# Kernel tuning notes

Hardware: AMD Instinct MI355X
Metric: run time of the kernel (lower is better)

## Reference

```python
import jax, jax.numpy as jnp
import numpy as np

EMB = 64
N_CONS = 100000
N_VARS = 200000
N_EDGES = 2000000


def _embed(x, shift, scale, W1, b1, W2, b2):
    # PreNormLayer (affine) -> Linear -> ReLU -> Linear -> ReLU
    x = (x - shift) * scale
    x = jax.nn.relu(x @ W1 + b1)
    return jax.nn.relu(x @ W2 + b2)


def _biconv(left, right, ei0, ei1, edge_lin, tgt_idx, n_tgt, tgt_feats,
            Wl, bl, Wr, sf, Wf, bf, sp, Woa, boa, Wob, bob):
    # gather-transform: per-edge joint features [E, EMB]
    joint = (left @ Wl + bl)[ei0] + edge_lin + (right @ Wr)[ei1]
    # feature_module_final: PreNorm(scale-only) -> ReLU -> Linear
    msg = jax.nn.relu(joint * sf) @ Wf + bf
    # scatter-add to target nodes, then post-conv PreNorm(scale-only)
    agg = jax.ops.segment_sum(msg, tgt_idx, num_segments=n_tgt) * sp
    h = jax.nn.relu(jnp.concatenate([agg, tgt_feats], axis=1) @ Woa + boa)
    return h @ Wob + bob


def _forward(constraint_features, edge_features, variable_features,
             c_shift, c_scale, c_W1, c_b1, c_W2, c_b2,
             v_shift, v_scale, v_W1, v_b1, v_W2, v_b2,
             e_shift, e_scale,
             vc_Wl, vc_bl, vc_We, vc_Wr, vc_sf, vc_Wf, vc_bf, vc_sp,
             vc_Woa, vc_boa, vc_Wob, vc_bob,
             cv_Wl, cv_bl, cv_We, cv_Wr, cv_sf, cv_Wf, cv_bf, cv_sp,
             cv_Woa, cv_boa, cv_Wob, cv_bob,
             out_W1, out_b1, out_W2, edge_indices):
    ei0, ei1 = edge_indices[0], edge_indices[1]
    c = _embed(constraint_features, c_shift, c_scale, c_W1, c_b1, c_W2, c_b2)
    v = _embed(variable_features, v_shift, v_scale, v_W1, v_b1, v_W2, v_b2)
    e = (edge_features - e_shift) * e_scale  # edge embedding = PreNorm only, dim 1
    # conv_v_to_c (right_to_left=True): target = constraints via ei0
    c = jax.nn.relu(_biconv(c, v, ei0, ei1, e @ vc_We, ei0, N_CONS, c,
                            vc_Wl, vc_bl, vc_Wr, vc_sf, vc_Wf, vc_bf, vc_sp,
                            vc_Woa, vc_boa, vc_Wob, vc_bob))
    # conv_c_to_v: target = variables via ei1
    v = jax.nn.relu(_biconv(c, v, ei0, ei1, e @ cv_We, ei1, N_VARS, v,
                            cv_Wl, cv_bl, cv_Wr, cv_sf, cv_Wf, cv_bf, cv_sp,
                            cv_Woa, cv_boa, cv_Wob, cv_bob))
    out = jax.nn.relu(v @ out_W1 + out_b1) @ out_W2  # [N_VARS, 1]
    return out.reshape(1, -1)


def setup_inputs():
    key = jax.random.key(0)
    ks = iter(jax.random.split(key, 64))

    def rn(shape, s=0.1):
        return (jax.random.normal(next(ks), shape, jnp.float32) * s).astype(jnp.float32)

    d = {}
    d["constraint_features"] = rn((N_CONS, 5), 1.0)
    d["edge_features"] = rn((N_EDGES, 1), 1.0)
    d["variable_features"] = rn((N_VARS, 19), 1.0)

    def prenorm(n, pre):
        d[pre + "shift"] = rn((n,), 0.05)
        d[pre + "scale"] = jnp.ones((n,), jnp.float32) + rn((n,), 0.05)

    prenorm(5, "c_"); prenorm(19, "v_"); prenorm(1, "e_")
    for pre, nin in (("c_", 5), ("v_", 19)):
        d[pre + "W1"] = rn((nin, EMB)); d[pre + "b1"] = rn((EMB,), 0.02)
        d[pre + "W2"] = rn((EMB, EMB)); d[pre + "b2"] = rn((EMB,), 0.02)
    for pre in ("vc_", "cv_"):
        d[pre + "Wl"] = rn((EMB, EMB)); d[pre + "bl"] = rn((EMB,), 0.02)
        d[pre + "We"] = rn((1, EMB)); d[pre + "Wr"] = rn((EMB, EMB))
        d[pre + "sf"] = jnp.float32(1.0) + rn((), 0.05)
        d[pre + "Wf"] = rn((EMB, EMB)); d[pre + "bf"] = rn((EMB,), 0.02)
        d[pre + "sp"] = jnp.float32(1.0) + rn((), 0.05)
        d[pre + "Woa"] = rn((2 * EMB, EMB)); d[pre + "boa"] = rn((EMB,), 0.02)
        d[pre + "Wob"] = rn((EMB, EMB)); d[pre + "bob"] = rn((EMB,), 0.02)
    d["out_W1"] = rn((EMB, EMB)); d["out_b1"] = rn((EMB,), 0.02)
    d["out_W2"] = rn((EMB, 1))
    d["edge_indices"] = jnp.stack([
        jax.random.randint(next(ks), (N_EDGES,), 0, N_CONS),
        jax.random.randint(next(ks), (N_EDGES,), 0, N_VARS)]).astype(jnp.int32)
    d["n_cons_per_sample"] = jnp.array([N_CONS], jnp.int32)
    d["n_vars_per_sample"] = jnp.array([N_VARS], jnp.int32)
    return d


def reference(constraint_features, edge_features, variable_features,
              c_shift, c_scale, c_W1, c_b1, c_W2, c_b2,
              v_shift, v_scale, v_W1, v_b1, v_W2, v_b2,
              e_shift, e_scale,
              vc_Wl, vc_bl, vc_We, vc_Wr, vc_sf, vc_Wf, vc_bf, vc_sp,
              vc_Woa, vc_boa, vc_Wob, vc_bob,
              cv_Wl, cv_bl, cv_We, cv_Wr, cv_sf, cv_Wf, cv_bf, cv_sp,
              cv_Woa, cv_boa, cv_Wob, cv_bob,
              out_W1, out_b1, out_W2,
              edge_indices, n_cons_per_sample, n_vars_per_sample):
    return _forward(constraint_features, edge_features, variable_features,
                    c_shift, c_scale, c_W1, c_b1, c_W2, c_b2,
                    v_shift, v_scale, v_W1, v_b1, v_W2, v_b2,
                    e_shift, e_scale,
                    vc_Wl, vc_bl, vc_We, vc_Wr, vc_sf, vc_Wf, vc_bf, vc_sp,
                    vc_Woa, vc_boa, vc_Wob, vc_bob,
                    cv_Wl, cv_bl, cv_We, cv_Wr, cv_sf, cv_Wf, cv_bf, cv_sp,
                    cv_Woa, cv_boa, cv_Wob, cv_bob,
                    out_W1, out_b1, out_W2, edge_indices)
```

## Files before the change

kernel.cpp:

```cpp
#include <hip/hip_runtime.h>
#include <hip/hip_bf16.h>

#define DEV __device__ __forceinline__

typedef __attribute__((ext_vector_type(8))) short short8;
typedef __attribute__((ext_vector_type(4))) float f32x4;

DEV unsigned short f2bf(float f) {
    __hip_bfloat16 h = __float2bfloat16(f);
    unsigned short u;
    __builtin_memcpy(&u, &h, 2);
    return u;
}
DEV float bf2f(unsigned short u) { return __uint_as_float((unsigned int)u << 16); }

DEV f32x4 mfma_bf16(short8 a, short8 b, f32x4 c) {
    return __builtin_amdgcn_mfma_f32_16x16x32_bf16(a, b, c, 0, 0, 0);
}

DEV void make_hilo(const float* a8, short8& hi, short8& lo) {
    #pragma unroll
    for (int j = 0; j < 8; ++j) {
        const float v = a8[j];
        const unsigned short h = f2bf(v);
        hi[j] = (short)h;
        lo[j] = (short)f2bf(v - bf2f(h));
    }
}

DEV void mfma3(f32x4 acc[4], short8 ah, short8 al,
               const unsigned short* __restrict__ Bh,
               const unsigned short* __restrict__ Bl,
               int nkt, int tidx, int lane) {
    #pragma unroll
    for (int c = 0; c < 4; ++c) {
        const size_t o = ((size_t)(c * nkt + tidx) * 64 + lane) * 8;
        const short8 bh = *(const short8*)(Bh + o);
        const short8 bl = *(const short8*)(Bl + o);
        acc[c] = mfma_bf16(ah, bh, acc[c]);
        acc[c] = mfma_bf16(al, bh, acc[c]);
        acc[c] = mfma_bf16(ah, bl, acc[c]);
    }
}

DEV int swf(int row, int col) {
    return row * 64 + ((((col >> 3) ^ row) & 7) << 3) + (col & 7);
}

DEV void gemm_lds(f32x4 acc[4], const float* Xl,
                  const unsigned short* Bh, const unsigned short* Bl,
                  int nkt, int t0, int ntk, int l15, int q, int lane) {
    for (int t = 0; t < ntk; ++t) {
        const int ch = (t * 4 + q) ^ (l15 & 7);
        const float* a8 = Xl + l15 * 64 + ch * 8;
        short8 ah, al;
        make_hilo(a8, ah, al);
        mfma3(acc, ah, al, Bh, Bl, nkt, t0 + t, lane);
    }
}

DEV void gemm_glb(f32x4 acc[4], const float* __restrict__ Xg, int rbase, int N,
                  const unsigned short* Bh, const unsigned short* Bl,
                  int nkt, int t0, int ntk, int l15, int q, int lane) {
    const int grow = rbase + l15;
    const bool ok = grow < N;
    for (int t = 0; t < ntk; ++t) {
        float a8[8];
        if (ok) {
            const float4 v0 = *(const float4*)(Xg + (size_t)grow * 64 + t * 32 + q * 8);
            const float4 v1 = *(const float4*)(Xg + (size_t)grow * 64 + t * 32 + q * 8 + 4);
            a8[0] = v0.x; a8[1] = v0.y; a8[2] = v0.z; a8[3] = v0.w;
            a8[4] = v1.x; a8[5] = v1.y; a8[6] = v1.z; a8[7] = v1.w;
        } else {
            #pragma unroll
            for (int j = 0; j < 8; ++j) a8[j] = 0.f;
        }
        short8 ah, al;
        make_hilo(a8, ah, al);
        mfma3(acc, ah, al, Bh, Bl, nkt, t0 + t, lane);
    }
}

#define NMAT 15
struct PrepArgs {
    const float* src[NMAT];
    unsigned short* hi[NMAT];
    unsigned short* lo[NMAT];
    int nkt[NMAT];
    int KR[NMAT];
};

__global__ __launch_bounds__(256)
void prep_kernel(PrepArgs pa)
{
    const int m = blockIdx.y;
    const int nkt = pa.nkt[m];
    const int nthr = nkt * 4 * 64;
    const int p = blockIdx.x * 256 + threadIdx.x;
    if (p >= nthr) return;
    const int f = p >> 6, l = p & 63;
    const int c = f / nkt, t = f % nkt;
    const int kbase = t * 32 + ((l >> 4) << 3);
    const int n = c * 16 + (l & 15);
    const float* W = pa.src[m];
    const int KR = pa.KR[m];
    unsigned short* ph = pa.hi[m] + (size_t)p * 8;
    unsigned short* pl = pa.lo[m] + (size_t)p * 8;
    #pragma unroll
    for (int j = 0; j < 8; ++j) {
        const int k = kbase + j;
        const float v = (k < KR) ? W[k * 64 + n] : 0.f;
        const unsigned short h = f2bf(v);
        ph[j] = h;
        pl[j] = f2bf(v - bf2f(h));
    }
}

struct FusedArgs {
    const int* ei; int E; int nH;
    int* h1; int* h2; unsigned int* rank;
    int tC, tV;
    const float* cf; int NC;
    const float* c_shift; const float* c_scale;
    const float* vf; int NV;
    const float* v_shift; const float* v_scale;
    const unsigned short *cW1h, *cW1l, *cW2h, *cW2l, *cWt1h, *cWt1l;
    const unsigned short *vW1h, *vW1l, *vW2h, *vW2l, *vWt1h, *vWt1l, *vWt2h, *vWt2l;
    const float *c_b1, *c_b2, *v_b1, *v_b2, *vc_bl;
    const float *vc_sf, *cv_sf;
    float* Emc; float* Emv;
    unsigned short* A1; unsigned short* B1; unsigned short* B2;
};

__global__ __launch_bounds__(256)
void fused_he_kernel(FusedArgs a)
{
    __shared__ __align__(16) float X0[4][16 * 32];
    __shared__ __align__(16) float Hb[4][1024];
    __shared__ __align__(16) float Eb[4][1024];

    const int half = blockIdx.x & 1;
    const int idx  = blockIdx.x >> 1;

    if (half == 0) {
        const int stride = a.nH * 256;
        for (int e = idx * 256 + (int)threadIdx.x; e < a.E; e += stride) {
            const int r1 = atomicAdd(a.h1 + a.ei[e], 1);
            const int r2 = atomicAdd(a.h2 + a.ei[a.E + e], 1);
            a.rank[e] = (unsigned int)r1 | ((unsigned int)r2 << 16);
        }
        return;
    }

    int tile = idx;
    const float* x; int N; int IN;
    const float *shift, *scale, *b1, *b2, *bt1;
    const unsigned short *W1h, *W1l, *W2h, *W2l, *Wt1h, *Wt1l;
    const unsigned short *Wt2h = nullptr, *Wt2l = nullptr;
    float* Em; unsigned short* T1; unsigned short* T2 = nullptr;
    float sf1, sf2 = 0.f;
    if (tile < a.tC) {
        x = a.cf; N = a.NC; IN = 5; shift = a.c_shift; scale = a.c_scale;
        W1h = a.cW1h; W1l = a.cW1l; b1 = a.c_b1;
        W2h = a.cW2h; W2l = a.cW2l; b2 = a.c_b2;
        Em = a.Emc; Wt1h = a.cWt1h; Wt1l = a.cWt1l; bt1 = a.vc_bl;
        sf1 = a.vc_sf[0]; T1 = a.A1;
    } else {
        tile -= a.tC;
        x = a.vf; N = a.NV; IN = 19; shift = a.v_shift; scale = a.v_scale;
        W1h = a.vW1h; W1l = a.vW1l; b1 = a.v_b1;
        W2h = a.vW2h; W2l = a.vW2l; b2 = a.v_b2;
        Em = a.Emv; Wt1h = a.vWt1h; Wt1l = a.vWt1l; bt1 = nullptr;
        sf1 = a.vc_sf[0]; T1 = a.B1;
        Wt2h = a.vWt2h; Wt2l = a.vWt2l; sf2 = a.cv_sf[0]; T2 = a.B2;
    }

    const int w = threadIdx.x >> 6, lane = threadIdx.x & 63;
    const int l15 = lane & 15, q = lane >> 4;
    const int rbase = tile * 64 + w * 16;

    #pragma unroll
    for (int i = 0; i < 8; ++i) {
        const int p = lane + 64 * i;
        const int row = p >> 5, col = p & 31;
        const int grow = rbase + row;
        float v = 0.f;
        if (grow < N && col < IN) v = (x[(size_t)grow * IN + col] - shift[col]) * scale[col];
        X0[w][row * 32 + (((col >> 3) ^ (row & 3)) << 3) + (col & 7)] = v;
    }

    {
        f32x4 acc[4] = {{0,0,0,0},{0,0,0,0},{0,0,0,0},{0,0,0,0}};
        const int ch = q ^ (l15 & 3);
        short8 ah, al;
        make_hilo(&X0[w][l15 * 32 + ch * 8], ah, al);
        mfma3(acc, ah, al, W1h, W1l, 1, 0, lane);
        #pragma unroll
        for (int c = 0; c < 4; ++c) {
            const int col = c * 16 + l15;
            const float bb = b1[col];
            #pragma unroll
            for (int r = 0; r < 4; ++r)
                Hb[w][swf(q * 4 + r, col)] = fmaxf(acc[c][r] + bb, 0.f);
        }
    }
    {
        f32x4 acc[4] = {{0,0,0,0},{0,0,0,0},{0,0,0,0},{0,0,0,0}};
        gemm_lds(acc, Hb[w], W2h, W2l, 2, 0, 2, l15, q, lane);
        #pragma unroll
        for (int c = 0; c < 4; ++c) {
            const int col = c * 16 + l15;
            const float bb = b2[col];
            #pragma unroll
            for (int r = 0; r < 4; ++r) {
                const int row = q * 4 + r;
                const int grow = rbase + row;
                const float v = fmaxf(acc[c][r] + bb, 0.f);
                Eb[w][swf(row, col)] = v;
                if (grow < N) Em[(size_t)grow * 64 + col] = v;
            }
        }
    }
    {
        f32x4 acc[4] = {{0,0,0,0},{0,0,0,0},{0,0,0,0},{0,0,0,0}};
        gemm_lds(acc, Eb[w], Wt1h, Wt1l, 2, 0, 2, l15, q, lane);
        #pragma unroll
        for (int c = 0; c < 4; ++c) {
            const int col = c * 16 + l15;
            const float bb = bt1 ? bt1[col] : 0.f;
            #pragma unroll
            for (int r = 0; r < 4; ++r) {
                const int grow = rbase + q * 4 + r;
                if (grow < N) T1[(size_t)grow * 64 + col] = f2bf(sf1 * (acc[c][r] + bb));
            }
        }
    }
    if (T2 != nullptr) {
        f32x4 acc[4] = {{0,0,0,0},{0,0,0,0},{0,0,0,0},{0,0,0,0}};
        gemm_lds(acc, Eb[w], Wt2h, Wt2l, 2, 0, 2, l15, q, lane);
        #pragma unroll
        for (int c = 0; c < 4; ++c) {
            const int col = c * 16 + l15;
            #pragma unroll
            for (int r = 0; r < 4; ++r) {
                const int grow = rbase + q * 4 + r;
                if (grow < N) T2[(size_t)grow * 64 + col] = f2bf(sf2 * acc[c][r]);
            }
        }
    }
}

template<bool IS_POST2>
__global__ __launch_bounds__(256)
void post_mfma(int N, const float* __restrict__ G, const int* __restrict__ rs,
               const float* __restrict__ Em,
               const unsigned short* __restrict__ Wfh, const unsigned short* __restrict__ Wfl,
               const float* __restrict__ bfv, const float* __restrict__ spp,
               const unsigned short* __restrict__ Woah, const unsigned short* __restrict__ Woal,
               const float* __restrict__ boa,
               const unsigned short* __restrict__ Wobh, const unsigned short* __restrict__ Wobl,
               const float* __restrict__ bob,
               const unsigned short* __restrict__ W4h, const unsigned short* __restrict__ W4l,
               const float* __restrict__ b4,
               const float* __restrict__ sf2p, unsigned short* __restrict__ A2,
               const float* __restrict__ oW2, float* __restrict__ out)
{
    __shared__ __align__(16) float BA[4][1024];
    __shared__ __align__(16) float BB[4][1024];

    const int w = threadIdx.x >> 6, lane = threadIdx.x & 63;
    const int l15 = lane & 15, q = lane >> 4;
    const float sp = spp[0];
    const float sf2 = IS_POST2 ? 0.f : sf2p[0];
    const int rbase = blockIdx.x * 64 + w * 16;

    {
        f32x4 acc[4] = {{0,0,0,0},{0,0,0,0},{0,0,0,0},{0,0,0,0}};
        gemm_glb(acc, G, rbase, N, Wfh, Wfl, 2, 0, 2, l15, q, lane);
        float dgr[4];
        #pragma unroll
        for (int r = 0; r < 4; ++r) {
            const int grow = rbase + q * 4 + r;
            dgr[r] = (grow < N) ? (float)(rs[grow + 1] - rs[grow]) : 0.f;
        }
        #pragma unroll
        for (int c = 0; c < 4; ++c) {
            const int col = c * 16 + l15;
            const float bb = bfv[col];
            #pragma unroll
            for (int r = 0; r < 4; ++r)
                BA[w][swf(q * 4 + r, col)] = (acc[c][r] + dgr[r] * bb) * sp;
        }
    }
    {
        f32x4 acc[4] = {{0,0,0,0},{0,0,0,0},{0,0,0,0},{0,0,0,0}};
        gemm_lds(acc, BA[w], Woah, Woal, 4, 0, 2, l15, q, lane);
        gemm_glb(acc, Em, rbase, N, Woah, Woal, 4, 2, 2, l15, q, lane);
        #pragma unroll
        for (int c = 0; c < 4; ++c) {
            const int col = c * 16 + l15;
            const float bb = boa[col];
            #pragma unroll
            for (int r = 0; r < 4; ++r)
                BB[w][swf(q * 4 + r, col)] = fmaxf(acc[c][r] + bb, 0.f);
        }
    }
    {
        f32x4 acc[4] = {{0,0,0,0},{0,0,0,0},{0,0,0,0},{0,0,0,0}};
        gemm_lds(acc, BB[w], Wobh, Wobl, 2, 0, 2, l15, q, lane);
        #pragma unroll
        for (int c = 0; c < 4; ++c) {
            const int col = c * 16 + l15;
            const float bb = bob[col];
            #pragma unroll
            for (int r = 0; r < 4; ++r)
                BA[w][swf(q * 4 + r, col)] = fmaxf(acc[c][r] + bb, 0.f);
        }
    }
    {
        f32x4 acc[4] = {{0,0,0,0},{0,0,0,0},{0,0,0,0},{0,0,0,0}};
        gemm_lds(acc, BA[w], W4h, W4l, 2, 0, 2, l15, q, lane);
        if (!IS_POST2) {
            #pragma unroll
            for (int c = 0; c < 4; ++c) {
                const int col = c * 16 + l15;
                const float bb = b4[col];
                #pragma unroll
                for (int r = 0; r < 4; ++r) {
                    const int grow = rbase + q * 4 + r;
                    if (grow < N) A2[(size_t)grow * 64 + col] = f2bf(sf2 * (acc[c][r] + bb));
                }
            }
        } else {
            float w2c[4], bb4[4];
            #pragma unroll
            for (int c = 0; c < 4; ++c) {
                const int col = c * 16 + l15;
                w2c[c] = oW2[col];
                bb4[c] = b4[col];
            }
            #pragma unroll
            for (int r = 0; r < 4; ++r) {
                float s = 0.f;
                #pragma unroll
                for (int c = 0; c < 4; ++c)
                    s += fmaxf(acc[c][r] + bb4[c], 0.f) * w2c[c];
                s += __shfl_xor(s, 1);
                s += __shfl_xor(s, 2);
                s += __shfl_xor(s, 4);
                s += __shfl_xor(s, 8);
                const int grow = rbase + q * 4 + r;
                if (l15 == 0 && grow < N) out[grow] = s;
            }
        }
    }
}

__global__ __launch_bounds__(256)
void scanA2_kernel(const int* __restrict__ h1, int n1, int* __restrict__ cs1,
                   const int* __restrict__ h2, int n2, int* __restrict__ cs2)
{
    __shared__ int wsum[4];
    const int which = blockIdx.y;
    const int* h = which ? h2 : h1;
    const int n = which ? n2 : n1;
    int* csum = which ? cs2 : cs1;
    if (blockIdx.x * 4096 >= n) return;

    const int t = threadIdx.x, lane = t & 63, wid = t >> 6;
    const int base = blockIdx.x * 4096 + t * 16;
    int s = 0;
    #pragma unroll
    for (int j = 0; j < 16; ++j) {
        const int idx = base + j;
        if (idx < n) s += h[idx];
    }
    #pragma unroll
    for (int d = 1; d < 64; d <<= 1) s += __shfl_xor(s, d);
    if (lane == 0) wsum[wid] = s;
    __syncthreads();
    if (t == 0) csum[blockIdx.x] = wsum[0] + wsum[1] + wsum[2] + wsum[3];
}

__global__ __launch_bounds__(256)
void scanB2_kernel(int* __restrict__ cs1, int nch1, int* __restrict__ rs1, int n1,
                   int* __restrict__ cs2, int nch2, int* __restrict__ rs2, int n2)
{
    __shared__ int wsum[4];
    const int which = blockIdx.x;
    int* csum = which ? cs2 : cs1;
    const int nchunks = which ? nch2 : nch1;
    int* rs = which ? rs2 : rs1;
    const int n = which ? n2 : n1;

    const int t = threadIdx.x, lane = t & 63, wid = t >> 6;
    const int v = (t < nchunks) ? csum[t] : 0;
    int x = v;
    #pragma unroll
    for (int d = 1; d < 64; d <<= 1) { int y = __shfl_up(x, d); if (lane >= d) x += y; }
    if (lane == 63) wsum[wid] = x;
    __syncthreads();
    int woff = 0;
    for (int i = 0; i < wid; ++i) woff += wsum[i];
    if (t < nchunks) csum[t] = woff + x - v;
    if (t == 0) rs[n] = wsum[0] + wsum[1] + wsum[2] + wsum[3];
}

__global__ __launch_bounds__(256)
void scanC2_kernel(const int* __restrict__ h1, int n1, const int* __restrict__ cs1,
                   int* __restrict__ rs1,
                   const int* __restrict__ h2, int n2, const int* __restrict__ cs2,
                   int* __restrict__ rs2)
{
    __shared__ int wsum[4];
    const int which = blockIdx.y;
    const int* h = which ? h2 : h1;
    const int n = which ? n2 : n1;
    const int* csum = which ? cs2 : cs1;
    int* rs = which ? rs2 : rs1;
    if (blockIdx.x * 4096 >= n) return;

    const int t = threadIdx.x, lane = t & 63, wid = t >> 6;
    const int base = blockIdx.x * 4096 + t * 16;
    int loc[16];
    int s = 0;
    #pragma unroll
    for (int j = 0; j < 16; ++j) {
        loc[j] = s;
        const int idx = base + j;
        if (idx < n) s += h[idx];
    }
    int x = s;
    #pragma unroll
    for (int d = 1; d < 64; d <<= 1) { int y = __shfl_up(x, d); if (lane >= d) x += y; }
    if (lane == 63) wsum[wid] = x;
    __syncthreads();
    int woff = 0;
    for (int i = 0; i < wid; ++i) woff += wsum[i];
    const int toff = csum[blockIdx.x] + woff + x - s;
    #pragma unroll
    for (int j = 0; j < 16; ++j) {
        const int idx = base + j;
        if (idx < n) rs[idx] = toff + loc[j];
    }
}

__global__ __launch_bounds__(256)
void scatter_kernel(const int* __restrict__ ei, int E,
                    const float* __restrict__ ef,
                    const float* __restrict__ eshp, const float* __restrict__ escp,
                    const unsigned int* __restrict__ rank,
                    const int* __restrict__ rs1, const int* __restrict__ rs2,
                    int2* __restrict__ pairs1, int2* __restrict__ pairs2)
{
    const int e = blockIdx.x * 256 + threadIdx.x;
    if (e >= E) return;
    const int i0 = ei[e];
    const int i1 = ei[E + e];
    const unsigned int rk = rank[e];
    const float en = (ef[e] - eshp[0]) * escp[0];
    const int enb = __float_as_int(en);
    const int pos1 = rs1[i0] + (int)(rk & 0xffffu);
    const int pos2 = rs2[i1] + (int)(rk >> 16);
    pairs1[pos1] = make_int2(i1, enb);
    pairs2[pos2] = make_int2(i0, enb);
}

__global__ __launch_bounds__(256)
void agg_kernel(int nrows, const int* __restrict__ rs,
                const int2* __restrict__ pairs,
                const unsigned short* __restrict__ Ttgt,
                const unsigned short* __restrict__ Tsrc,
                const float* __restrict__ We, const float* __restrict__ sfp,
                float* __restrict__ G)
{
    const int r = threadIdx.x >> 6;
    const int j = threadIdx.x & 63;
    const int row = blockIdx.x * 4 + r;
    if (row >= nrows) return;

    const float base = bf2f(Ttgt[(size_t)row * 64 + j]);
    const float sfWe = sfp[0] * We[j];
    const int s = rs[row];
    const int e = rs[row + 1];

    float acc = 0.f;
    int p = s;
    for (; p + 1 < e; p += 2) {
        const int2 pr0 = pairs[p];
        const int2 pr1 = pairs[p + 1];
        const float bs0 = bf2f(Tsrc[(size_t)pr0.x * 64 + j]);
        const float bs1 = bf2f(Tsrc[(size_t)pr1.x * 64 + j]);
        acc += fmaxf(base + bs0 + __int_as_float(pr0.y) * sfWe, 0.f);
        acc += fmaxf(base + bs1 + __int_as_float(pr1.y) * sfWe, 0.f);
    }
    if (p < e) {
        const int2 pr = pairs[p];
        const float bs = bf2f(Tsrc[(size_t)pr.x * 64 + j]);
        acc += fmaxf(base + bs + __int_as_float(pr.y) * sfWe, 0.f);
    }
    G[(size_t)row * 64 + j] = acc;
}

extern "C" void kernel_launch(void* const* d_in, const int* in_sizes, int n_in,
                              void* d_out, int out_size, void* d_ws, size_t ws_size,
                              hipStream_t stream)
{
    const float* cf      = (const float*)d_in[0];
    const float* ef      = (const float*)d_in[1];
    const float* vf      = (const float*)d_in[2];
    const float* c_shift = (const float*)d_in[3];
    const float* c_scale = (const float*)d_in[4];
    const float* v_shift = (const float*)d_in[5];
    const float* v_scale = (const float*)d_in[6];
    const float* e_shift = (const float*)d_in[7];
    const float* e_scale = (const float*)d_in[8];
    const float* c_W1 = (const float*)d_in[9];
    const float* c_b1 = (const float*)d_in[10];
    const float* c_W2 = (const float*)d_in[11];
    const float* c_b2 = (const float*)d_in[12];
    const float* v_W1 = (const float*)d_in[13];
    const float* v_b1 = (const float*)d_in[14];
    const float* v_W2 = (const float*)d_in[15];
    const float* v_b2 = (const float*)d_in[16];
    const float* vc_Wl  = (const float*)d_in[17];
    const float* vc_bl  = (const float*)d_in[18];
    const float* vc_We  = (const float*)d_in[19];
    const float* vc_Wr  = (const float*)d_in[20];
    const float* vc_sf  = (const float*)d_in[21];
    const float* vc_Wf  = (const float*)d_in[22];
    const float* vc_bf  = (const float*)d_in[23];
    const float* vc_sp  = (const float*)d_in[24];
    const float* vc_Woa = (const float*)d_in[25];
    const float* vc_boa = (const float*)d_in[26];
    const float* vc_Wob = (const float*)d_in[27];
    const float* vc_bob = (const float*)d_in[28];
    const float* cv_Wl  = (const float*)d_in[29];
    const float* cv_bl  = (const float*)d_in[30];
    const float* cv_We  = (const float*)d_in[31];
    const float* cv_Wr  = (const float*)d_in[32];
    const float* cv_sf  = (const float*)d_in[33];
    const float* cv_Wf  = (const float*)d_in[34];
    const float* cv_bf  = (const float*)d_in[35];
    const float* cv_sp  = (const float*)d_in[36];
    const float* cv_Woa = (const float*)d_in[37];
    const float* cv_boa = (const float*)d_in[38];
    const float* cv_Wob = (const float*)d_in[39];
    const float* cv_bob = (const float*)d_in[40];
    const float* out_W1 = (const float*)d_in[41];
    const float* out_b1 = (const float*)d_in[42];
    const float* out_W2 = (const float*)d_in[43];
    const int*   eidx   = (const int*)d_in[44];

    const int NC = in_sizes[0] / 5;
    const int NV = in_sizes[2] / 19;
    const int E  = in_sizes[1];

    char* ws = (char*)d_ws;
    size_t off = 0;
    auto alloc = [&](size_t bytes) -> size_t {
        size_t o = off;
        off = (off + bytes + 255) & ~(size_t)255;
        return o;
    };
    size_t o_h1 = alloc((size_t)NC * 4);
    size_t o_h2 = alloc((size_t)NV * 4);
    size_t zero_bytes = off;
    size_t o_rs1  = alloc((size_t)(NC + 1) * 4);
    size_t o_rs2  = alloc((size_t)(NV + 1) * 4);
    size_t o_cs1  = alloc(256 * 4);
    size_t o_cs2  = alloc(256 * 4);
    size_t o_p1   = alloc((size_t)E * 8);
    size_t o_p2   = alloc((size_t)E * 8);
    size_t o_G1   = alloc((size_t)NC * 64 * 4);
    size_t o_G2   = alloc((size_t)NV * 64 * 4);
    size_t o_Emc  = alloc((size_t)NC * 64 * 4);
    size_t o_Emv  = alloc((size_t)NV * 64 * 4);
    size_t o_A1   = alloc((size_t)NC * 64 * 2);
    size_t o_B1   = alloc((size_t)NV * 64 * 2);
    size_t o_B2   = alloc((size_t)NV * 64 * 2);

    static const int nkt_arr[NMAT] = {1,2,2,1,2,2,2,2,4,2,2,2,4,2,2};
    static const int KR_arr[NMAT]  = {5,64,64,19,64,64,64,64,128,64,64,64,128,64,64};
    const float* src_arr[NMAT] = {c_W1, c_W2, vc_Wl, v_W1, v_W2, vc_Wr, cv_Wr,
                                  vc_Wf, vc_Woa, vc_Wob, cv_Wl,
                                  cv_Wf, cv_Woa, cv_Wob, out_W1};
    size_t o_wh[NMAT], o_wl[NMAT];
    for (int m = 0; m < NMAT; ++m) {
        o_wh[m] = alloc((size_t)nkt_arr[m] * 4 * 64 * 8 * 2);
        o_wl[m] = alloc((size_t)nkt_arr[m] * 4 * 64 * 8 * 2);
    }
    (void)ws_size; (void)n_in; (void)out_size;

    int*  h1   = (int*)(ws + o_h1);
    int*  h2   = (int*)(ws + o_h2);
    int*  rs1  = (int*)(ws + o_rs1);
    int*  rs2  = (int*)(ws + o_rs2);
    int*  cs1  = (int*)(ws + o_cs1);
    int*  cs2  = (int*)(ws + o_cs2);
    unsigned int* rank = (unsigned int*)(ws + o_G1);
    int2* p1   = (int2*)(ws + o_p1);
    int2* p2   = (int2*)(ws + o_p2);
    float* G1  = (float*)(ws + o_G1);
    float* G2  = (float*)(ws + o_G2);
    float* Emc = (float*)(ws + o_Emc);
    float* Emv = (float*)(ws + o_Emv);
    unsigned short* A1 = (unsigned short*)(ws + o_A1);
    unsigned short* B1 = (unsigned short*)(ws + o_B1);
    unsigned short* A2 = (unsigned short*)(ws + o_A1);
    unsigned short* B2 = (unsigned short*)(ws + o_B2);

    PrepArgs pa;
    for (int m = 0; m < NMAT; ++m) {
        pa.src[m] = src_arr[m];
        pa.hi[m] = (unsigned short*)(ws + o_wh[m]);
        pa.lo[m] = (unsigned short*)(ws + o_wl[m]);
        pa.nkt[m] = nkt_arr[m];
        pa.KR[m] = KR_arr[m];
    }
    auto WH = [&](int m) { return (const unsigned short*)(ws + o_wh[m]); };
    auto WL = [&](int m) { return (const unsigned short*)(ws + o_wl[m]); };

    hipMemsetAsync(ws, 0, zero_bytes, stream);

    prep_kernel<<<dim3(4, NMAT), 256, 0, stream>>>(pa);

    const int tC = (NC + 63) >> 6, tV = (NV + 63) >> 6;
    const int nE = tC + tV;
    FusedArgs fa;
    fa.ei = eidx; fa.E = E; fa.nH = nE;
    fa.h1 = h1; fa.h2 = h2; fa.rank = rank;
    fa.tC = tC; fa.tV = tV;
    fa.cf = cf; fa.NC = NC; fa.c_shift = c_shift; fa.c_scale = c_scale;
    fa.vf = vf; fa.NV = NV; fa.v_shift = v_shift; fa.v_scale = v_scale;
    fa.cW1h = WH(0); fa.cW1l = WL(0); fa.cW2h = WH(1); fa.cW2l = WL(1);
    fa.cWt1h = WH(2); fa.cWt1l = WL(2);
    fa.vW1h = WH(3); fa.vW1l = WL(3); fa.vW2h = WH(4); fa.vW2l = WL(4);
    fa.vWt1h = WH(5); fa.vWt1l = WL(5); fa.vWt2h = WH(6); fa.vWt2l = WL(6);
    fa.c_b1 = c_b1; fa.c_b2 = c_b2; fa.v_b1 = v_b1; fa.v_b2 = v_b2;
    fa.vc_bl = vc_bl; fa.vc_sf = vc_sf; fa.cv_sf = cv_sf;
    fa.Emc = Emc; fa.Emv = Emv; fa.A1 = A1; fa.B1 = B1; fa.B2 = B2;
    fused_he_kernel<<<2 * nE, 256, 0, stream>>>(fa);

    const int nch1 = (NC + 4095) / 4096, nch2 = (NV + 4095) / 4096;
    const int nchm = nch1 > nch2 ? nch1 : nch2;
    scanA2_kernel<<<dim3(nchm, 2), 256, 0, stream>>>(h1, NC, cs1, h2, NV, cs2);
    scanB2_kernel<<<2, 256, 0, stream>>>(cs1, nch1, rs1, NC, cs2, nch2, rs2, NV);
    scanC2_kernel<<<dim3(nchm, 2), 256, 0, stream>>>(h1, NC, cs1, rs1, h2, NV, cs2, rs2);

    scatter_kernel<<<(E + 255) / 256, 256, 0, stream>>>(
        eidx, E, ef, e_shift, e_scale, rank, rs1, rs2, p1, p2);

    agg_kernel<<<(NC + 3) / 4, 256, 0, stream>>>(
        NC, rs1, p1, A1, B1, vc_We, vc_sf, G1);
    post_mfma<false><<<tC, 256, 0, stream>>>(
        NC, G1, rs1, Emc,
        WH(7), WL(7), vc_bf, vc_sp,
        WH(8), WL(8), vc_boa,
        WH(9), WL(9), vc_bob,
        WH(10), WL(10), cv_bl,
        cv_sf, A2, nullptr, nullptr);

    agg_kernel<<<(NV + 3) / 4, 256, 0, stream>>>(
        NV, rs2, p2, B2, A2, cv_We, cv_sf, G2);
    post_mfma<true><<<tV, 256, 0, stream>>>(
        NV, G2, rs2, Emv,
        WH(11), WL(11), cv_bf, cv_sp,
        WH(12), WL(12), cv_boa,
        WH(13), WL(13), cv_bob,
        WH(14), WL(14), out_b1,
        nullptr, nullptr, out_W2, (float*)d_out);
}
```

Baseline: 813.3 us.

## Split edge scatter and overlap second-direction scatter with first aggregation

```diff
diff --git a/kernel.cpp b/kernel.cpp
--- a/kernel.cpp
+++ b/kernel.cpp
@@ -135,9 +135,7 @@
 __global__ __launch_bounds__(256)
 void fused_he_kernel(FusedArgs a)
 {
-    __shared__ __align__(16) float X0[4][16 * 32];
-    __shared__ __align__(16) float Hb[4][1024];
-    __shared__ __align__(16) float Eb[4][1024];
+    __shared__ __align__(16) float Bb[4][1024];
 
     const int half = blockIdx.x & 1;
     const int idx  = blockIdx.x >> 1;
@@ -179,21 +177,19 @@
     const int l15 = lane & 15, q = lane >> 4;
     const int rbase = tile * 64 + w * 16;
 
-    #pragma unroll
-    for (int i = 0; i < 8; ++i) {
-        const int p = lane + 64 * i;
-        const int row = p >> 5, col = p & 31;
-        const int grow = rbase + row;
-        float v = 0.f;
-        if (grow < N && col < IN) v = (x[(size_t)grow * IN + col] - shift[col]) * scale[col];
-        X0[w][row * 32 + (((col >> 3) ^ (row & 3)) << 3) + (col & 7)] = v;
-    }
-
     {
         f32x4 acc[4] = {{0,0,0,0},{0,0,0,0},{0,0,0,0},{0,0,0,0}};
-        const int ch = q ^ (l15 & 3);
+        const int grow = rbase + l15;
+        float a8[8];
+        #pragma unroll
+        for (int j = 0; j < 8; ++j) {
+            const int col = q * 8 + j;
+            float v = 0.f;
+            if (grow < N && col < IN) v = (x[(size_t)grow * IN + col] - shift[col]) * scale[col];
+            a8[j] = v;
+        }
         short8 ah, al;
-        make_hilo(&X0[w][l15 * 32 + ch * 8], ah, al);
+        make_hilo(a8, ah, al);
         mfma3(acc, ah, al, W1h, W1l, 1, 0, lane);
         #pragma unroll
         for (int c = 0; c < 4; ++c) {
@@ -201,12 +197,12 @@
             const float bb = b1[col];
             #pragma unroll
             for (int r = 0; r < 4; ++r)
-                Hb[w][swf(q * 4 + r, col)] = fmaxf(acc[c][r] + bb, 0.f);
+                Bb[w][swf(q * 4 + r, col)] = fmaxf(acc[c][r] + bb, 0.f);
         }
     }
     {
         f32x4 acc[4] = {{0,0,0,0},{0,0,0,0},{0,0,0,0},{0,0,0,0}};
-        gemm_lds(acc, Hb[w], W2h, W2l, 2, 0, 2, l15, q, lane);
+        gemm_lds(acc, Bb[w], W2h, W2l, 2, 0, 2, l15, q, lane);
         #pragma unroll
         for (int c = 0; c < 4; ++c) {
             const int col = c * 16 + l15;
@@ -216,14 +212,14 @@
                 const int row = q * 4 + r;
                 const int grow = rbase + row;
                 const float v = fmaxf(acc[c][r] + bb, 0.f);
-                Eb[w][swf(row, col)] = v;
+                Bb[w][swf(row, col)] = v;
                 if (grow < N) Em[(size_t)grow * 64 + col] = v;
             }
         }
     }
     {
         f32x4 acc[4] = {{0,0,0,0},{0,0,0,0},{0,0,0,0},{0,0,0,0}};
-        gemm_lds(acc, Eb[w], Wt1h, Wt1l, 2, 0, 2, l15, q, lane);
+        gemm_lds(acc, Bb[w], Wt1h, Wt1l, 2, 0, 2, l15, q, lane);
         #pragma unroll
         for (int c = 0; c < 4; ++c) {
             const int col = c * 16 + l15;
@@ -237,7 +233,7 @@
     }
     if (T2 != nullptr) {
         f32x4 acc[4] = {{0,0,0,0},{0,0,0,0},{0,0,0,0},{0,0,0,0}};
-        gemm_lds(acc, Eb[w], Wt2h, Wt2l, 2, 0, 2, l15, q, lane);
+        gemm_lds(acc, Bb[w], Wt2h, Wt2l, 2, 0, 2, l15, q, lane);
         #pragma unroll
         for (int c = 0; c < 4; ++c) {
             const int col = c * 16 + l15;
@@ -446,44 +442,32 @@
 }
 
 __global__ __launch_bounds__(256)
-void scatter_kernel(const int* __restrict__ ei, int E,
-                    const float* __restrict__ ef,
-                    const float* __restrict__ eshp, const float* __restrict__ escp,
-                    const unsigned int* __restrict__ rank,
-                    const int* __restrict__ rs1, const int* __restrict__ rs2,
-                    int2* __restrict__ pairs1, int2* __restrict__ pairs2)
+void scatter1_kernel(const int* __restrict__ ei, int E,
+                     const float* __restrict__ ef,
+                     const float* __restrict__ eshp, const float* __restrict__ escp,
+                     const unsigned int* __restrict__ rank,
+                     const int* __restrict__ rs1, int2* __restrict__ pairs1)
 {
     const int e = blockIdx.x * 256 + threadIdx.x;
     if (e >= E) return;
     const int i0 = ei[e];
     const int i1 = ei[E + e];
-    const unsigned int rk = rank[e];
     const float en = (ef[e] - eshp[0]) * escp[0];
-    const int enb = __float_as_int(en);
-    const int pos1 = rs1[i0] + (int)(rk & 0xffffu);
-    const int pos2 = rs2[i1] + (int)(rk >> 16);
-    pairs1[pos1] = make_int2(i1, enb);
-    pairs2[pos2] = make_int2(i0, enb);
-}
-
-__global__ __launch_bounds__(256)
-void agg_kernel(int nrows, const int* __restrict__ rs,
-                const int2* __restrict__ pairs,
-                const unsigned short* __restrict__ Ttgt,
-                const unsigned short* __restrict__ Tsrc,
-                const float* __restrict__ We, const float* __restrict__ sfp,
-                float* __restrict__ G)
-{
-    const int r = threadIdx.x >> 6;
-    const int j = threadIdx.x & 63;
-    const int row = blockIdx.x * 4 + r;
-    if (row >= nrows) return;
-
+    const int pos1 = rs1[i0] + (int)(rank[e] & 0xffffu);
+    pairs1[pos1] = make_int2(i1, __float_as_int(en));
+}
+
+DEV void agg_body(int row, int j, const int* __restrict__ rs,
+                  const int2* __restrict__ pairs,
+                  const unsigned short* __restrict__ Ttgt,
+                  const unsigned short* __restrict__ Tsrc,
+                  const float* __restrict__ We, const float* __restrict__ sfp,
+                  float* __restrict__ G)
+{
     const float base = bf2f(Ttgt[(size_t)row * 64 + j]);
     const float sfWe = sfp[0] * We[j];
     const int s = rs[row];
     const int e = rs[row + 1];
-
     float acc = 0.f;
     int p = s;
     for (; p + 1 < e; p += 2) {
@@ -500,6 +484,51 @@
         acc += fmaxf(base + bs + __int_as_float(pr.y) * sfWe, 0.f);
     }
     G[(size_t)row * 64 + j] = acc;
+}
+
+__global__ __launch_bounds__(256)
+void fused_s2a1_kernel(const int* __restrict__ ei, int E,
+                       const float* __restrict__ ef,
+                       const float* __restrict__ eshp, const float* __restrict__ escp,
+                       const unsigned int* __restrict__ rank,
+                       const int* __restrict__ rs2, int2* __restrict__ pairs2,
+                       int nS,
+                       int NC, const int* __restrict__ rs1,
+                       const int2* __restrict__ pairs1,
+                       const unsigned short* __restrict__ A1,
+                       const unsigned short* __restrict__ B1,
+                       const float* __restrict__ We, const float* __restrict__ sfp,
+                       float* __restrict__ G1)
+{
+    const int half = blockIdx.x & 1;
+    const int idx  = blockIdx.x >> 1;
+    if (half == 0) {
+        if (idx >= nS) return;
+        const int e = idx * 256 + (int)threadIdx.x;
+        if (e >= E) return;
+        const int i0 = ei[e];
+        const int i1 = ei[E + e];
+        const float en = (ef[e] - eshp[0]) * escp[0];
+        const int pos2 = rs2[i1] + (int)(rank[e] >> 16);
+        pairs2[pos2] = make_int2(i0, __float_as_int(en));
+    } else {
+        const int row = idx * 4 + (int)(threadIdx.x >> 6);
+        if (row >= NC) return;
+        agg_body(row, (int)(threadIdx.x & 63), rs1, pairs1, A1, B1, We, sfp, G1);
+    }
+}
+
+__global__ __launch_bounds__(256)
+void agg_kernel(int nrows, const int* __restrict__ rs,
+                const int2* __restrict__ pairs,
+                const unsigned short* __restrict__ Ttgt,
+                const unsigned short* __restrict__ Tsrc,
+                const float* __restrict__ We, const float* __restrict__ sfp,
+                float* __restrict__ G)
+{
+    const int row = blockIdx.x * 4 + (int)(threadIdx.x >> 6);
+    if (row >= nrows) return;
+    agg_body(row, (int)(threadIdx.x & 63), rs, pairs, Ttgt, Tsrc, We, sfp, G);
 }
 
 extern "C" void kernel_launch(void* const* d_in, const int* in_sizes, int n_in,
@@ -598,7 +627,7 @@
     int*  rs2  = (int*)(ws + o_rs2);
     int*  cs1  = (int*)(ws + o_cs1);
     int*  cs2  = (int*)(ws + o_cs2);
-    unsigned int* rank = (unsigned int*)(ws + o_G1);
+    unsigned int* rank = (unsigned int*)(ws + o_G2);
     int2* p1   = (int2*)(ws + o_p1);
     int2* p2   = (int2*)(ws + o_p2);
     float* G1  = (float*)(ws + o_G1);
@@ -648,11 +677,16 @@
     scanB2_kernel<<<2, 256, 0, stream>>>(cs1, nch1, rs1, NC, cs2, nch2, rs2, NV);
     scanC2_kernel<<<dim3(nchm, 2), 256, 0, stream>>>(h1, NC, cs1, rs1, h2, NV, cs2, rs2);
 
-    scatter_kernel<<<(E + 255) / 256, 256, 0, stream>>>(
-        eidx, E, ef, e_shift, e_scale, rank, rs1, rs2, p1, p2);
-
-    agg_kernel<<<(NC + 3) / 4, 256, 0, stream>>>(
+    scatter1_kernel<<<(E + 255) / 256, 256, 0, stream>>>(
+        eidx, E, ef, e_shift, e_scale, rank, rs1, p1);
+
+    const int nS = (E + 255) / 256;
+    const int nA1 = (NC + 3) / 4;
+    const int M = nS > nA1 ? nS : nA1;
+    fused_s2a1_kernel<<<2 * M, 256, 0, stream>>>(
+        eidx, E, ef, e_shift, e_scale, rank, rs2, p2, nS,
         NC, rs1, p1, A1, B1, vc_We, vc_sf, G1);
+
     post_mfma<false><<<tC, 256, 0, stream>>>(
         NC, G1, rs1, Emc,
         WH(7), WL(7), vc_bf, vc_sp,
```

Result: no change. 822.5 us (+1.1%).
